# Optimization experiments

Measured on AMD Instinct MI355X. Metric: run time of the kernel, lower is better.

The kernel has to match this reference:

```python
import jax, jax.numpy as jnp
import numpy as np

BETA = 0.9      # LIF leak
THRESH = 1.0    # snntorch Leaky default threshold
SLOPE = 25.0    # fast_sigmoid surrogate slope

@jax.custom_vjp
def spike(x):
    # Heaviside forward, fast_sigmoid surrogate backward
    return (x > 0).astype(x.dtype)

def _spike_fwd(x):
    return spike(x), x

def _spike_bwd(x, g):
    return (g / (SLOPE * jnp.abs(x) + 1.0) ** 2,)

spike.defvjp(_spike_fwd, _spike_bwd)


def setup_inputs() -> dict:
    key = jax.random.key(0)
    k0, k1, k2, k3, k4 = jax.random.split(key, 5)
    B, T, I, H, C = 256, 100, 512, 1024, 8
    x = jax.random.normal(k0, (B, T, I), dtype=jnp.float32)
    s1 = 1.0 / np.sqrt(I)
    s2 = 1.0 / np.sqrt(H)
    W1 = jax.random.uniform(k1, (H, I), jnp.float32, -s1, s1)
    b1 = jax.random.uniform(k2, (H,), jnp.float32, -s1, s1)
    W2 = jax.random.uniform(k3, (C, H), jnp.float32, -s2, s2)
    b2 = jax.random.uniform(k4, (C,), jnp.float32, -s2, s2)
    return {"x": x, "W1": W1, "b1": b1, "W2": W2, "b2": b2}


def reference(x, W1, b1, W2, b2):
    # x: [B, T, I]
    B, T, I = x.shape
    H = W1.shape[0]
    # fc1 for all timesteps as one big GEMM (same math as per-step loop).
    cur = jnp.einsum('bti,hi->tbh', x, W1) + b1  # [T, B, H]

    def step(mem, c):
        # snntorch Leaky (reset_mechanism='subtract'):
        reset = spike(mem - THRESH)
        mem_new = BETA * mem + c - reset * THRESH
        spk = spike(mem_new - THRESH)
        return mem_new, spk

    mem0 = jnp.zeros((B, H), dtype=x.dtype)
    _, spk_rec = jax.lax.scan(step, mem0, cur)  # spk_rec: [T, B, H]

    # sum_t (spk_t @ W2.T + b2) == (sum_t spk_t) @ W2.T + T*b2
    spk_sum = spk_rec.sum(axis=0)  # [B, H]
    logits = spk_sum @ W2.T + T * b2  # [B, C]
    return logits
```

## Files before the change

kernel.cpp:

```cpp
#include <hip/hip_runtime.h>


#define B_   256
#define T_   100
#define I_   512
#define H_   1024
#define C_   8
#define M_   (B_ * T_)
#define KS_  1024
#define SC   64.0f
#define ISC  (1.0f / 4096.0f)

typedef _Float16 half8 __attribute__((ext_vector_type(8)));
typedef float floatx16 __attribute__((ext_vector_type(16)));

__device__ __forceinline__ void ld_g2l(const _Float16* g, _Float16* l) {
    __builtin_amdgcn_global_load_lds(
        (const __attribute__((address_space(1))) void*)g,
        (__attribute__((address_space(3))) void*)l, 16, 0, 0);
}

__global__ void __launch_bounds__(256)
split_all(const float* __restrict__ x, const float* __restrict__ W1,
          const float* __restrict__ b2, _Float16* __restrict__ Asp,
          float* __restrict__ out) {
    int g = blockIdx.x * 256 + threadIdx.x;
    if (g < B_ * C_) out[g] = 100.0f * b2[g & (C_ - 1)];
    int row = g >> 6;
    int i0 = (g & 63) * 8;
    const float* src = (row < M_) ? (x + (size_t)row * I_ + i0)
                                  : (W1 + (size_t)(row - M_) * I_ + i0);
    float4 v0 = *(const float4*)(src);
    float4 v1 = *(const float4*)(src + 4);
    float vv[8] = {v0.x, v0.y, v0.z, v0.w, v1.x, v1.y, v1.z, v1.w};
    half8 hi, lo;
#pragma unroll
    for (int j = 0; j < 8; ++j) {
        float s = vv[j] * SC;
        _Float16 h = (_Float16)s;
        hi[j] = h;
        lo[j] = (_Float16)(s - (float)h);
    }
    _Float16* r = Asp + (size_t)row * KS_ + i0;
    *(half8*)(r) = hi;
    *(half8*)(r + 512) = lo;
}

#define MFMA32(A, Bv, Cacc) \
    Cacc = __builtin_amdgcn_mfma_f32_32x32x16_f16(A, Bv, Cacc, 0, 0, 0)

#define STAGE(dd, koff) do {                                         \
    _Float16* lb = &sm.buf[0][0] + (dd) * 8192 + w * 512;            \
    ld_g2l(gah + (koff), lb);                                        \
    ld_g2l(gal + (koff), lb + 2048);                                 \
    ld_g2l(gbh + (koff), lb + 4096);                                 \
    ld_g2l(gbl + (koff), lb + 6144);                                 \
} while (0)

#define COMPUTE(dd) do {                                             \
    const _Float16* bb = &sm.buf[0][0] + (dd) * 8192;                \
    half8 ah[2], al[2], bh[2], bl[2];                                \
    _Pragma("unroll")                                                \
    for (int f = 0; f < 2; ++f) {                                    \
        ah[f] = *(const half8*)(bb + ra + f * 512);                  \
        al[f] = *(const half8*)(bb + 2048 + ra + f * 512);           \
        bh[f] = *(const half8*)(bb + 4096 + rb + f * 512);           \
        bl[f] = *(const half8*)(bb + 6144 + rb + f * 512);           \
    }                                                                \
    _Pragma("unroll")                                                \
    for (int fm = 0; fm < 2; ++fm) {                                 \
        _Pragma("unroll")                                            \
        for (int fn = 0; fn < 2; ++fn) {                             \
            MFMA32(ah[fm], bh[fn], acc[fm][fn]);                     \
            MFMA32(ah[fm], bl[fn], acc[fm][fn]);                     \
            MFMA32(al[fm], bh[fn], acc[fm][fn]);                     \
        }                                                            \
    }                                                                \
} while (0)

__global__ void __launch_bounds__(256, 2)
snn_mfma(const _Float16* __restrict__ Asp, const _Float16* __restrict__ Wsp,
         const float* __restrict__ b1, const float* __restrict__ W2,
         float* __restrict__ logits) {
    __shared__ union {
        __align__(16) _Float16 buf[2][8192];
        float Cs[32 * 128];
    } sm;
    const int tid = threadIdx.x;
    const int lane = tid & 63;
    const int w = tid >> 6;

    const int xcd = blockIdx.x & 7;
    const int jj = blockIdx.x >> 3;
    const int b  = xcd * 32 + (jj >> 3);
    const int n0 = (jj & 7) * 128;

    const int wm = (w >> 1) * 64;
    const int wn = (w & 1) * 64;
    const int l31 = lane & 31;
    const int q2 = lane >> 5;

    const int lp = lane ^ ((lane >> 3) & 7);
    const int rl = lp >> 1;
    const int cl8 = (lp & 1) * 8;
    const _Float16* gah = Asp + (size_t)(b * T_ + w * 32 + rl) * KS_ + cl8;
    const _Float16* gal = gah + 512;
    const _Float16* gbh = Wsp + (size_t)(n0 + w * 32 + rl) * KS_ + cl8;
    const _Float16* gbl = gbh + 512;

    const int swz = ((l31 >> 2) & 7) << 3;
    const int ra = ((wm + l31) * 16 + q2 * 8) ^ swz;
    const int rb = ((wn + l31) * 16 + q2 * 8) ^ swz;

    floatx16 acc[2][2];
#pragma unroll
    for (int i = 0; i < 2; ++i)
#pragma unroll
        for (int j = 0; j < 2; ++j)
#pragma unroll
            for (int e = 0; e < 16; ++e) acc[i][j][e] = 0.f;

    STAGE(0, 0);
#pragma unroll 2
    for (int c = 0; c < 31; ++c) {
        const int d = c & 1;
        STAGE(d ^ 1, (c + 1) * 16);
        asm volatile("s_waitcnt vmcnt(4)" ::: "memory");
        __builtin_amdgcn_s_barrier();
        COMPUTE(d);
        __builtin_amdgcn_s_barrier();
        asm volatile("" ::: "memory");
    }
    asm volatile("s_waitcnt vmcnt(0)" ::: "memory");
    __builtin_amdgcn_s_barrier();
    COMPUTE(1);
    __syncthreads();

    float b1c[2];
#pragma unroll
    for (int fn = 0; fn < 2; ++fn) b1c[fn] = b1[n0 + wn + fn * 32 + l31];

    float mem = 0.f, ss = 0.f;

#pragma unroll
    for (int p = 0; p < 4; ++p) {
        const int fm = p & 1;
        if ((w >> 1) == (p >> 1)) {
#pragma unroll
            for (int r = 0; r < 16; ++r) {
                const int row = (r & 3) + 8 * (r >> 2) + 4 * q2;
                float* dst = &sm.Cs[row * 128 + wn + l31];
#pragma unroll
                for (int fn = 0; fn < 2; ++fn)
                    dst[fn * 32] = acc[fm][fn][r] * ISC + b1c[fn];
            }
        }
        __syncthreads();
        if (tid < 128) {
            const int nt = (p == 3) ? 4 : 32;
#pragma unroll 8
            for (int t = 0; t < nt; ++t) {
                float cv = sm.Cs[t * 128 + tid];
                float reset = (mem > 1.0f) ? 1.0f : 0.0f;
                mem = 0.9f * mem + cv - reset;
                ss += (mem > 1.0f) ? 1.0f : 0.0f;
            }
        }
        __syncthreads();
    }

    if (tid < 128) {
#pragma unroll
        for (int cc = 0; cc < C_; ++cc) {
            float v = ss * W2[cc * H_ + n0 + tid];
#pragma unroll
            for (int off = 32; off; off >>= 1) v += __shfl_down(v, off, 64);
            if (lane == 0) atomicAdd(&logits[b * C_ + cc], v);
        }
    }
}

extern "C" void kernel_launch(void* const* d_in, const int* in_sizes, int n_in,
                              void* d_out, int out_size, void* d_ws, size_t ws_size,
                              hipStream_t stream) {
    const float* x  = (const float*)d_in[0];
    const float* W1 = (const float*)d_in[1];
    const float* b1 = (const float*)d_in[2];
    const float* W2 = (const float*)d_in[3];
    const float* b2 = (const float*)d_in[4];
    float* out = (float*)d_out;

    char* ws = (char*)d_ws;
    _Float16* Asp = (_Float16*)ws;
    _Float16* Wsp = (_Float16*)(ws + (size_t)M_ * KS_ * 2);

    hipLaunchKernelGGL(split_all, dim3((M_ + H_) * 64 / 256), dim3(256), 0, stream,
                       x, W1, b2, Asp, out);
    hipLaunchKernelGGL(snn_mfma, dim3(B_ * 8), dim3(256), 0, stream,
                       Asp, Wsp, b1, W2, out);
}
```

Before: 240.4 us.

## Store split fp16 operands in contiguous 32-row panel tiles for coalesced staging

The conversion kernel now writes the hi/lo fp16 halves of x and W1 into a panel layout. Each 32-row by 16-column cell occupies a contiguous 512-element block, with the hi and lo halves of a panel kept in separate 16K regions. The GEMM kernel's global-to-LDS loads then read one contiguous 1 KB chunk per wave per stage instead of 32 strided row segments, which aims to improve DRAM/L2 access efficiency. The gain is better coalescing, and the cost is more involved index arithmetic. There is also a dead, convoluted isA expression left in the code.

```diff
diff --git a/kernel.cpp b/kernel.cpp
--- a/kernel.cpp
+++ b/kernel.cpp
@@ -7,9 +7,12 @@
 #define H_   1024
 #define C_   8
 #define M_   (B_ * T_)
-#define KS_  1024
 #define SC   64.0f
 #define ISC  (1.0f / 4096.0f)
+
+#define CELL_  512
+#define SHALF_ 16384
+#define PANEL_ 32768
 
 typedef _Float16 half8 __attribute__((ext_vector_type(8)));
 typedef float floatx16 __attribute__((ext_vector_type(16)));
@@ -24,12 +27,20 @@
 split_all(const float* __restrict__ x, const float* __restrict__ W1,
           const float* __restrict__ b2, _Float16* __restrict__ Asp,
           float* __restrict__ out) {
-    int g = blockIdx.x * 256 + threadIdx.x;
+    const int tid = threadIdx.x;
+    const int lane = tid & 63;
+    int g = blockIdx.x * 256 + tid;
     if (g < B_ * C_) out[g] = 100.0f * b2[g & (C_ - 1)];
-    int row = g >> 6;
-    int i0 = (g & 63) * 8;
-    const float* src = (row < M_) ? (x + (size_t)row * I_ + i0)
-                                  : (W1 + (size_t)(row - M_) * I_ + i0);
+
+    const int W = blockIdx.x * 4 + (tid >> 6);
+    const bool isA = (W < M_ / 32 * 32 / 32 * 1 * 32 * 32 / 32 ? (W < 800 * 32) : false);
+    const int Wl = (W < 25600) ? W : (W - 25600);
+    const int p = Wl >> 5;
+    const int c = Wl & 31;
+    const int r = p * 32 + (lane >> 1);
+    const int col = c * 16 + (lane & 1) * 8;
+    const float* src = (W < 25600) ? (x + (size_t)r * I_ + col)
+                                   : (W1 + (size_t)r * I_ + col);
     float4 v0 = *(const float4*)(src);
     float4 v1 = *(const float4*)(src + 4);
     float vv[8] = {v0.x, v0.y, v0.z, v0.w, v1.x, v1.y, v1.z, v1.w};
@@ -41,20 +52,21 @@
         hi[j] = h;
         lo[j] = (_Float16)(s - (float)h);
     }
-    _Float16* r = Asp + (size_t)row * KS_ + i0;
-    *(half8*)(r) = hi;
-    *(half8*)(r + 512) = lo;
+    _Float16* base = Asp + ((W < 25600) ? 0 : (size_t)800 * PANEL_);
+    _Float16* d = base + (size_t)p * PANEL_ + c * CELL_ + lane * 8;
+    *(half8*)(d) = hi;
+    *(half8*)(d + SHALF_) = lo;
 }
 
 #define MFMA32(A, Bv, Cacc) \
     Cacc = __builtin_amdgcn_mfma_f32_32x32x16_f16(A, Bv, Cacc, 0, 0, 0)
 
-#define STAGE(dd, koff) do {                                         \
+#define STAGE(dd, cc) do {                                           \
     _Float16* lb = &sm.buf[0][0] + (dd) * 8192 + w * 512;            \
-    ld_g2l(gah + (koff), lb);                                        \
-    ld_g2l(gal + (koff), lb + 2048);                                 \
-    ld_g2l(gbh + (koff), lb + 4096);                                 \
-    ld_g2l(gbl + (koff), lb + 6144);                                 \
+    ld_g2l(gah + (cc) * CELL_, lb);                                  \
+    ld_g2l(gal + (cc) * CELL_, lb + 2048);                           \
+    ld_g2l(gbh + (cc) * CELL_, lb + 4096);                           \
+    ld_g2l(gbl + (cc) * CELL_, lb + 6144);                           \
 } while (0)
 
 #define COMPUTE(dd) do {                                             \
@@ -101,12 +113,14 @@
     const int q2 = lane >> 5;
 
     const int lp = lane ^ ((lane >> 3) & 7);
-    const int rl = lp >> 1;
-    const int cl8 = (lp & 1) * 8;
-    const _Float16* gah = Asp + (size_t)(b * T_ + w * 32 + rl) * KS_ + cl8;
-    const _Float16* gal = gah + 512;
-    const _Float16* gbh = Wsp + (size_t)(n0 + w * 32 + rl) * KS_ + cl8;
-    const _Float16* gbl = gbh + 512;
+    const int ra_row = b * T_ + w * 32 + (lp >> 1);
+    const int rb_row = n0 + w * 32 + (lp >> 1);
+    const _Float16* gah = Asp + (size_t)(ra_row >> 5) * PANEL_
+                              + (ra_row & 31) * 16 + (lp & 1) * 8;
+    const _Float16* gal = gah + SHALF_;
+    const _Float16* gbh = Wsp + (size_t)(rb_row >> 5) * PANEL_
+                              + (rb_row & 31) * 16 + (lp & 1) * 8;
+    const _Float16* gbl = gbh + SHALF_;
 
     const int swz = ((l31 >> 2) & 7) << 3;
     const int ra = ((wm + l31) * 16 + q2 * 8) ^ swz;
@@ -124,7 +138,7 @@
 #pragma unroll 2
     for (int c = 0; c < 31; ++c) {
         const int d = c & 1;
-        STAGE(d ^ 1, (c + 1) * 16);
+        STAGE(d ^ 1, c + 1);
         asm volatile("s_waitcnt vmcnt(4)" ::: "memory");
         __builtin_amdgcn_s_barrier();
         COMPUTE(d);
@@ -192,9 +206,9 @@
 
     char* ws = (char*)d_ws;
     _Float16* Asp = (_Float16*)ws;
-    _Float16* Wsp = (_Float16*)(ws + (size_t)M_ * KS_ * 2);
-
-    hipLaunchKernelGGL(split_all, dim3((M_ + H_) * 64 / 256), dim3(256), 0, stream,
+    _Float16* Wsp = Asp + (size_t)800 * PANEL_;
+
+    hipLaunchKernelGGL(split_all, dim3(6656), dim3(256), 0, stream,
                        x, W1, b2, Asp, out);
     hipLaunchKernelGGL(snn_mfma, dim3(B_ * 8), dim3(256), 0, stream,
                        Asp, Wsp, b1, W2, out);
```

Measured after the change: 198.7 us. 17.4% less time.
